# Optimization experiments

Measured on AMD Instinct MI355X. Metric: run time of the kernel, lower is better.

The kernel has to match this reference:

```python
import jax, jax.numpy as jnp
import numpy as np


def setup_inputs() -> dict:
    key = jax.random.key(0)
    N, H, W = 2, 64, 64
    C = (2 * H - 1) * (2 * W - 1)  # relative-position mask channels
    x = jax.random.normal(key, (N, C, H, W), dtype=jnp.float32)
    return {"x": x}


def reference(x):
    # PSA 'collect': out[n, i*W + j, h, w] = x[n, (i-h+H-1)*(2W-1) + (j-w+W-1), h, w]
    # Every (i, j, h, w) combination yields a valid relative index, so this is a
    # pure gather along the channel axis with per-pixel-varying indices.
    N, _, H, W = x.shape
    i = jnp.arange(H)[:, None, None, None]  # output row i
    j = jnp.arange(W)[None, :, None, None]  # output col j
    h = jnp.arange(H)[None, None, :, None]  # feature row h
    w = jnp.arange(W)[None, None, None, :]  # feature col w
    rel = (i - h + (H - 1)) * (2 * W - 1) + (j - w + (W - 1))  # [H, W, H, W]
    idx = jnp.broadcast_to(rel.reshape(1, H * W, H, W), (N, H * W, H, W))
    out = jnp.take_along_axis(x, idx, axis=1)  # [N, H*W, H, W]
    return out
```

## Files before the change

kernel.cpp:

```cpp
#include <hip/hip_runtime.h>


#define H_ 64
#define W_ 64
#define C_ 16129
#define RW_ 127
#define TS_ 68

__global__ __launch_bounds__(256, 8) void collect_kernel(const float* __restrict__ x,
                                                         float* __restrict__ out) {
    __shared__ float tile[H_ * TS_];

    const int b = blockIdx.x;
    const int n = b >> 12;
    const int h = (b >> 6) & 63;
    const int i = b & 63;
    const int dr = i - h + 63;

    const int t = threadIdx.x;

    const float* __restrict__ src =
        x + (((size_t)n * C_ + (size_t)dr * RW_) * H_ + h) * W_;

    #pragma unroll
    for (int k = 0; k < 8; ++k) {
        const int idx = t + k * 256;
        if (idx < RW_ * 16) {
            const int cc = idx >> 4;
            const int s4 = idx & 15;
            const int w0 = max(0, 63 - cc);
            const int w1 = min(63, 126 - cc);
            if (s4 >= (w0 >> 2) && s4 <= (w1 >> 2)) {
                const float4 v =
                    *reinterpret_cast<const float4*>(src + cc * (H_ * W_) + s4 * 4);
                const int jb = cc + s4 * 4 - 63;
                const float* vf = reinterpret_cast<const float*>(&v);
                #pragma unroll
                for (int e = 0; e < 4; ++e) {
                    const int j = jb + e;
                    if ((unsigned)j < (unsigned)H_) {
                        tile[j * TS_ + s4 * 4 + e] = vf[e];
                    }
                }
            }
        }
    }
    __syncthreads();

    const int w4 = t & 15;
    const int j0 = t >> 4;
    float* __restrict__ dstbase =
        out + (((size_t)n * (H_ * W_) + (size_t)i * W_) * H_ + h) * W_ + w4 * 4;

    #pragma unroll
    for (int k = 0; k < 4; ++k) {
        const int j = j0 + k * 16;
        *reinterpret_cast<float4*>(dstbase + (size_t)j * (H_ * W_)) =
            *reinterpret_cast<const float4*>(&tile[j * TS_ + w4 * 4]);
    }
}

extern "C" void kernel_launch(void* const* d_in, const int* in_sizes, int n_in,
                              void* d_out, int out_size, void* d_ws, size_t ws_size,
                              hipStream_t stream) {
    const float* x = (const float*)d_in[0];
    float* out = (float*)d_out;
    collect_kernel<<<dim3(8192), dim3(256), 0, stream>>>(x, out);
}
```

Baseline: 76.48 us.

## Process four feature rows per block to write contiguous 1KB output runs

```diff
diff --git a/kernel.cpp b/kernel.cpp
--- a/kernel.cpp
+++ b/kernel.cpp
@@ -5,41 +5,47 @@
 #define W_ 64
 #define C_ 16129
 #define RW_ 127
-#define TS_ 68
+#define G_ 4
+#define TS_ 260
 
-__global__ __launch_bounds__(256, 8) void collect_kernel(const float* __restrict__ x,
+__global__ __launch_bounds__(512, 4) void collect_kernel(const float* __restrict__ x,
                                                          float* __restrict__ out) {
     __shared__ float tile[H_ * TS_];
 
-    const int b = blockIdx.x;
-    const int n = b >> 12;
-    const int h = (b >> 6) & 63;
-    const int i = b & 63;
-    const int dr = i - h + 63;
+    const int b  = blockIdx.x;
+    const int n  = b >> 10;
+    const int i  = (b >> 4) & 63;
+    const int hq = b & 15;
+    const int h0 = hq * G_;
+    const int D0 = i + 63 - h0;
 
     const int t = threadIdx.x;
 
-    const float* __restrict__ src =
-        x + (((size_t)n * C_ + (size_t)dr * RW_) * H_ + h) * W_;
+    const float* __restrict__ basen = x + (size_t)n * C_ * (H_ * W_);
 
     #pragma unroll
-    for (int k = 0; k < 8; ++k) {
-        const int idx = t + k * 256;
-        if (idx < RW_ * 16) {
-            const int cc = idx >> 4;
-            const int s4 = idx & 15;
+    for (int k = 0; k < 16; ++k) {
+        const int idx = t + (k << 9);
+        const int hp  = idx >> 11;
+        const int rem = idx & 2047;
+        if (rem < RW_ * 16) {
+            const int cc = rem >> 4;
+            const int s4 = rem & 15;
             const int w0 = max(0, 63 - cc);
             const int w1 = min(63, 126 - cc);
             if (s4 >= (w0 >> 2) && s4 <= (w1 >> 2)) {
-                const float4 v =
-                    *reinterpret_cast<const float4*>(src + cc * (H_ * W_) + s4 * 4);
+                const float* src = basen
+                    + (size_t)(D0 - hp) * (RW_ * H_ * W_)
+                    + (size_t)cc * (H_ * W_)
+                    + (h0 + hp) * W_ + s4 * 4;
+                const float4 v = *reinterpret_cast<const float4*>(src);
                 const int jb = cc + s4 * 4 - 63;
                 const float* vf = reinterpret_cast<const float*>(&v);
                 #pragma unroll
                 for (int e = 0; e < 4; ++e) {
                     const int j = jb + e;
                     if ((unsigned)j < (unsigned)H_) {
-                        tile[j * TS_ + s4 * 4 + e] = vf[e];
+                        tile[j * TS_ + (hp << 6) + s4 * 4 + e] = vf[e];
                     }
                 }
             }
@@ -47,16 +53,16 @@
     }
     __syncthreads();
 
-    const int w4 = t & 15;
-    const int j0 = t >> 4;
-    float* __restrict__ dstbase =
-        out + (((size_t)n * (H_ * W_) + (size_t)i * W_) * H_ + h) * W_ + w4 * 4;
-
+    const int j  = t >> 3;
+    const int s0 = t & 7;
+    float* __restrict__ dst =
+        out + ((size_t)(n * (H_ * W_) + i * W_ + j) << 12) + (h0 << 6);
+    const float* __restrict__ trow = &tile[j * TS_];
     #pragma unroll
-    for (int k = 0; k < 4; ++k) {
-        const int j = j0 + k * 16;
-        *reinterpret_cast<float4*>(dstbase + (size_t)j * (H_ * W_)) =
-            *reinterpret_cast<const float4*>(&tile[j * TS_ + w4 * 4]);
+    for (int k = 0; k < 8; ++k) {
+        const int slot = s0 + (k << 3);
+        *reinterpret_cast<float4*>(dst + slot * 4) =
+            *reinterpret_cast<const float4*>(trow + slot * 4);
     }
 }
 
@@ -65,5 +71,5 @@
                               hipStream_t stream) {
     const float* x = (const float*)d_in[0];
     float* out = (float*)d_out;
-    collect_kernel<<<dim3(8192), dim3(256), 0, stream>>>(x, out);
+    collect_kernel<<<dim3(2048), dim3(512), 0, stream>>>(x, out);
 }
```

Measured after the change: 84.24 us. +10.1%, slower.
